# Optimization experiments

Measured on AMD Instinct MI355X. Metric: run time of the kernel, lower is better.

The kernel has to match this reference:

```python
import jax, jax.numpy as jnp
import numpy as np

KEEP_ATTN = 0.9   # 1 - attn_pdrop
KEEP_RESID = 0.9  # 1 - resid_pdrop
B, T, C, H = 2, 2048, 1024, 16


def setup_inputs() -> dict:
    key = jax.random.key(0)
    ks = jax.random.split(key, 5)
    x = jax.random.normal(ks[0], (B, T, C), jnp.float32)
    Wqkv = jax.random.normal(ks[1], (C, 3 * C), jnp.float32) / np.float32(np.sqrt(C))
    bqkv = jnp.zeros((3 * C,), jnp.float32)
    Wproj = jax.random.normal(ks[2], (C, C), jnp.float32) / np.float32(np.sqrt(C))
    bproj = jnp.zeros((C,), jnp.float32)
    # dropout keep-masks (replace the attn_pdrop_key / resid_pdrop_key args)
    attn_drop_mask = jax.random.bernoulli(ks[3], KEEP_ATTN, (B, H, T, T))
    resid_drop_mask = jax.random.bernoulli(ks[4], KEEP_RESID, (B, T, C))
    return dict(x=x, Wqkv=Wqkv, bqkv=bqkv, Wproj=Wproj, bproj=bproj,
                attn_drop_mask=attn_drop_mask, resid_drop_mask=resid_drop_mask)


def reference(x, Wqkv, bqkv, Wproj, bproj, attn_drop_mask, resid_drop_mask):
    Bx, Tx, Cx = x.shape
    Hh = attn_drop_mask.shape[1]
    hd = Cx // Hh  # head_dim
    qkv = x @ Wqkv + bqkv                              # [B,T,3C]
    q, k, v = jnp.split(qkv, 3, axis=-1)
    q = q.reshape(Bx, Tx, Hh, hd).swapaxes(1, 2)       # [B,H,T,hd]
    k = k.reshape(Bx, Tx, Hh, hd).swapaxes(1, 2)
    v = v.reshape(Bx, Tx, Hh, hd).swapaxes(1, 2)
    attn = jnp.einsum('bhqd,bhkd->bhqk', q, k) / np.float32(np.sqrt(hd))  # [B,H,T,T]
    causal = jnp.tril(jnp.ones((Tx, Tx), dtype=bool))  # lower-triangular bias
    attn = jnp.where(causal, attn, -jnp.inf)
    attn = jax.nn.softmax(attn, axis=-1)
    attn = jnp.where(attn_drop_mask, attn / np.float32(KEEP_ATTN), 0.0)
    y = jnp.einsum('bhqk,bhkd->bhqd', attn, v)         # [B,H,T,hd]
    y = y.swapaxes(1, 2).reshape(Bx, Tx, Cx)           # [B,T,C]
    y = y @ Wproj + bproj
    y = jnp.where(resid_drop_mask, y / np.float32(KEEP_RESID), 0.0)
    return y
```

## Files before the change

kernel.cpp:

```cpp
#include <hip/hip_runtime.h>
#include <cstdint>
#include <cstddef>

typedef unsigned int u32;
typedef unsigned short u16;
typedef short s8v __attribute__((ext_vector_type(8)));
typedef __bf16 bf8v __attribute__((ext_vector_type(8)));
typedef float f4v __attribute__((ext_vector_type(4)));

#define B_ 2
#define T_ 2048
#define C_ 1024
#define H_ 16
#define HD 64
#define LOG2E 1.4426950408889634f
#define SCL (0.125f * LOG2E)

__device__ __forceinline__ u16 f2bf(float f){
  u32 u = __builtin_bit_cast(u32, f);
  u += 0x7fffu + ((u >> 16) & 1u);
  return (u16)(u >> 16);
}

__device__ __forceinline__ f4v mfma16(s8v a, s8v b, f4v c){
  return __builtin_amdgcn_mfma_f32_16x16x32_bf16((bf8v)a, (bf8v)b, c, 0, 0, 0);
}

__device__ __forceinline__ void gload_lds16(const void* g, void* l){
  __builtin_amdgcn_global_load_lds((const __attribute__((address_space(1))) u32*)g,
                                   (__attribute__((address_space(3))) u32*)l,
                                   16, 0, 0);
}

__device__ __forceinline__ void barrier_keep16(){
  asm volatile("s_waitcnt vmcnt(16) lgkmcnt(0)\n\ts_barrier" ::: "memory");
}

__global__ __launch_bounds__(256) void cast_bf16_k(const float* __restrict__ in,
                                                   u16* __restrict__ out, int n8){
  int i = blockIdx.x * 256 + threadIdx.x;
  if (i >= n8) return;
  const float4* p = (const float4*)in;
  float4 a = p[i*2], b = p[i*2+1];
  uint4 o = make_uint4(
     (u32)f2bf(a.x) | ((u32)f2bf(a.y) << 16),
     (u32)f2bf(a.z) | ((u32)f2bf(a.w) << 16),
     (u32)f2bf(b.x) | ((u32)f2bf(b.y) << 16),
     (u32)f2bf(b.z) | ((u32)f2bf(b.w) << 16));
  ((uint4*)out)[i] = o;
}

__global__ __launch_bounds__(256) void tcast_k(const float* __restrict__ src,
                                               u16* __restrict__ dst, int R, int C){
  __shared__ u16 tile[64][65];
  int t = threadIdx.x;
  int c0 = blockIdx.x * 64, r0 = blockIdx.y * 64;
  int col = t & 63, rb = t >> 6;
#pragma unroll
  for (int i = 0; i < 16; i++){
    int row = rb + i*4;
    tile[row][col] = f2bf(src[(size_t)(r0+row)*C + (c0+col)]);
  }
  __syncthreads();
#pragma unroll
  for (int i = 0; i < 16; i++){
    int oc = rb + i*4;
    dst[(size_t)(c0+oc)*R + (r0+col)] = tile[col][oc];
  }
}

__global__ __launch_bounds__(256) void tv_k(const u16* __restrict__ qkv,
                                            u16* __restrict__ VT){
  __shared__ u16 tile[64][65];
  int t = threadIdx.x;
  int tt = blockIdx.x, bh = blockIdx.y;
  int b = bh >> 4, h = bh & 15;
  int col = t & 63, rb = t >> 6;
  const u16* src = qkv + (size_t)(b*T_ + tt*64)*(3*C_) + 2*C_ + h*HD;
#pragma unroll
  for (int i = 0; i < 16; i++){
    int row = rb + i*4;
    tile[row][col] = src[(size_t)row*(3*C_) + col];
  }
  __syncthreads();
  u16* dst = VT + (size_t)bh*HD*T_ + tt*64;
#pragma unroll
  for (int i = 0; i < 16; i++){
    int d = rb + i*4;
    dst[(size_t)d*T_ + col] = tile[col][d];
  }
}

template<int MODE>
__global__ __launch_bounds__(256) void gemm_k(const u16* __restrict__ A,
                        const u16* __restrict__ Bt,
                        const float* __restrict__ bias, void* __restrict__ outp,
                        const int* __restrict__ rmask,
                        int M, int N, int K){
  __shared__ __align__(16) u16 As[2][128*32];
  __shared__ __align__(16) u16 Bs[2][128*32];
  int t = threadIdx.x;
  int w = t >> 6, l = t & 63;
  int lo = l & 15, lg = l >> 4;
  int m0 = blockIdx.x * 128, n0 = blockIdx.y * 128;
  int wm = (w >> 1) * 64, wn = (w & 1) * 64;

  auto STAGE = [&](int buf, int ks){
#pragma unroll
    for (int i = 0; i < 2; i++){
      int c = t + i*256;
      int row = c >> 2, k8 = (c & 3) * 8;
      gload_lds16(A  + (size_t)(m0+row)*K + ks + k8,
                  (char*)As[buf] + (size_t)(w*64 + i*256)*16);
      gload_lds16(Bt + (size_t)(n0+row)*K + ks + k8,
                  (char*)Bs[buf] + (size_t)(w*64 + i*256)*16);
    }
  };

  f4v acc[4][4];
#pragma unroll
  for (int i=0;i<4;i++)
#pragma unroll
    for (int j=0;j<4;j++) acc[i][j] = (f4v){0.f,0.f,0.f,0.f};

  STAGE(0, 0);
  __syncthreads();
  int cur = 0;
  for (int ks = 0; ks < K; ks += 32){
    if (ks + 32 < K) STAGE(cur ^ 1, ks + 32);
    s8v af[4], bfr[4];
#pragma unroll
    for (int mt=0; mt<4; mt++)
      af[mt]  = *(const s8v*)(&As[cur][0] + (wm + mt*16 + lo)*32 + lg*8);
#pragma unroll
    for (int nt=0; nt<4; nt++)
      bfr[nt] = *(const s8v*)(&Bs[cur][0] + (wn + nt*16 + lo)*32 + lg*8);
#pragma unroll
    for (int mt=0; mt<4; mt++)
#pragma unroll
      for (int nt=0; nt<4; nt++)
        acc[mt][nt] = mfma16(af[mt], bfr[nt], acc[mt][nt]);
    __syncthreads();
    cur ^= 1;
  }

#pragma unroll
  for (int mt=0; mt<4; mt++){
#pragma unroll
    for (int nt=0; nt<4; nt++){
#pragma unroll
      for (int r=0; r<4; r++){
        int row = m0 + wm + mt*16 + lg*4 + r;
        int col = n0 + wn + nt*16 + lo;
        float v = acc[mt][nt][r] + bias[col];
        if (MODE == 0){
          ((u16*)outp)[(size_t)row*N + col] = f2bf(v);
        } else {
          float o = rmask[(size_t)row*N + col] ? v * (1.0f/0.9f) : 0.0f;
          ((float*)outp)[(size_t)row*N + col] = o;
        }
      }
    }
  }
}

__global__ __launch_bounds__(256, 4) void attn_k(const u16* __restrict__ qkv,
                        const u16* __restrict__ VT,
                        const int* __restrict__ amask,
                        u16* __restrict__ Y){
  __shared__ __align__(16) u16 Ks[2][64*64];
  __shared__ __align__(16) u16 Vs[2][64*64];
  __shared__ __align__(16) u16 Ps[4][16*64];
  const int t = threadIdx.x;
  const int w = t >> 6, l = t & 63;
  const int lo = l & 15, lg = l >> 4;

  const int n = blockIdx.x;
  const int bh = n & 31;
  const int j = n >> 5, a = j & 7, bb = j >> 3;
  const int qt = (bb & 1) ? (31 - a - 8*(bb >> 1)) : (a + 8*(bb >> 1));
  const int b = bh >> 4, h = bh & 15;
  const int q0 = qt * 64;
  const int qmaxw = q0 + w*16 + 15;

  const u16* Kg = qkv + (size_t)(b*T_)*(3*C_) + C_ + h*HD;
  const u16* Vg = VT + (size_t)bh*HD*T_;
  const int* mg = amask + (size_t)bh*T_*T_ + (size_t)(q0 + w*16)*T_;

  int qrow = q0 + w*16 + lo;
  const u16* qp = qkv + (size_t)(b*T_ + qrow)*(3*C_) + h*HD;
  s8v qf0 = *(const s8v*)(qp + lg*8);
  s8v qf1 = *(const s8v*)(qp + 32 + lg*8);

  f4v acc[4];
#pragma unroll
  for (int i=0;i<4;i++) acc[i] = (f4v){0.f,0.f,0.f,0.f};
  float lsum[4] = {0.f, 0.f, 0.f, 0.f};

  auto STAGE = [&](int buf, int kt){
#pragma unroll
    for (int i = 0; i < 2; i++){
      int c = t + i*256;
      int row = c >> 3;
      int cc = (c & 7) ^ (row & 7);
      gload_lds16(Kg + (size_t)(kt*64 + row)*(3*C_) + cc*8,
                  (char*)Ks[buf] + (size_t)(w*64 + i*256)*16);
      gload_lds16(Vg + (size_t)row*T_ + kt*64 + cc*8,
                  (char*)Vs[buf] + (size_t)(w*64 + i*256)*16);
    }
    __builtin_amdgcn_sched_barrier(0);
  };

  auto MLOAD = [&](int kt, int* m){
#pragma unroll
    for (int k4 = 0; k4 < 4; k4++)
#pragma unroll
      for (int r = 0; r < 4; r++)
        m[k4*4 + r] = mg[(size_t)(lg*4 + r)*T_ + kt*64 + k4*16 + lo];
  };

  auto TILE = [&](int kt, int cur, const int* m, bool diag){
    const char* kb = (const char*)Ks[cur];
    const char* vb = (const char*)Vs[cur];
    char* pw = (char*)&Ps[w][0];
#pragma unroll
    for (int k4 = 0; k4 < 4; k4++){
      bool active = !diag || (kt*64 + k4*16 <= qmaxw);
      f4v s = (f4v){0.f,0.f,0.f,0.f};
      if (active){
#pragma unroll
        for (int kk = 0; kk < 2; kk++){
          int krow = k4*16 + lo;
          int off = krow*128 + (((kk*4 + lg) ^ (krow & 7)) << 4);
          s8v kf = *(const s8v*)(kb + off);
          s = mfma16(kk ? qf1 : qf0, kf, s);
        }
      }
      int kidx = kt*64 + k4*16 + lo;
#pragma unroll
      for (int r=0;r<4;r++){
        float sv = active ? s[r] : -1e30f;
        if (diag){
          int qi = q0 + w*16 + lg*4 + r;
          sv = (kidx <= qi) ? sv : -1e30f;
        }
        float e = exp2f(sv * SCL);
        lsum[r] += e;
        u16 pv = m[k4*4 + r] ? f2bf(e) : (u16)0;
        int prow = lg*4 + r;
        int off = (prow*128 + (k4*16 + lo)*2) ^ ((prow & 7) << 4);
        *(u16*)(pw + off) = pv;
      }
    }
    s8v pf[2];
#pragma unroll
    for (int kk=0;kk<2;kk++){
      int off = lo*128 + (((kk*4 + lg) ^ (lo & 7)) << 4);
      pf[kk] = *(const s8v*)(pw + off);
    }
#pragma unroll
    for (int dt=0; dt<4; dt++){
#pragma unroll
      for (int kk=0; kk<2; kk++){
        int vrow = dt*16 + lo;
        int voff = vrow*128 + (((kk*4 + lg) ^ (vrow & 7)) << 4);
        s8v vf = *(const s8v*)(vb + voff);
        acc[dt] = mfma16(pf[kk], vf, acc[dt]);
      }
    }
  };

  int mA[16], mB[16];
  STAGE(0, 0);
  MLOAD(0, mA);
  __syncthreads();

  int cur = 0;
  int kt = 0;
  for (; kt + 1 < qt; kt += 2){
    STAGE(cur ^ 1, kt + 1);
    MLOAD(kt + 1, mB);
    TILE(kt, cur, mA, false);
    barrier_keep16();
    cur ^= 1;

    STAGE(cur ^ 1, kt + 2);
    MLOAD(kt + 2, mA);
    TILE(kt + 1, cur, mB, false);
    barrier_keep16();
    cur ^= 1;
  }
  if (kt < qt){
    STAGE(cur ^ 1, kt + 1);
    MLOAD(kt + 1, mB);
    TILE(kt, cur, mA, false);
    barrier_keep16();
    cur ^= 1;
    TILE(qt, cur, mB, true);
  } else {
    TILE(qt, cur, mA, true);
  }

#pragma unroll
  for (int r=0;r<4;r++){
    float v = lsum[r];
    v += __shfl_xor(v, 1);
    v += __shfl_xor(v, 2);
    v += __shfl_xor(v, 4);
    v += __shfl_xor(v, 8);
    int qi = q0 + w*16 + lg*4 + r;
    float inv = 1.0f / (v * 0.9f);
    u16* yp = Y + (size_t)(b*T_ + qi)*C_ + h*HD;
#pragma unroll
    for (int dt=0; dt<4; dt++){
      yp[dt*16 + lo] = f2bf(acc[dt][r] * inv);
    }
  }
}

extern "C" void kernel_launch(void* const* d_in, const int* in_sizes, int n_in,
                              void* d_out, int out_size, void* d_ws, size_t ws_size,
                              hipStream_t stream){
  const float* x     = (const float*)d_in[0];
  const float* Wqkv  = (const float*)d_in[1];
  const float* bqkv  = (const float*)d_in[2];
  const float* Wproj = (const float*)d_in[3];
  const float* bproj = (const float*)d_in[4];
  const int* amask = (const int*)d_in[5];
  const int* rmask = (const int*)d_in[6];
  float* out = (float*)d_out;

  char* ws = (char*)d_ws;
  u16* xb     = (u16*)(ws);
  u16* WqkvT  = (u16*)(ws + (size_t)( 8<<20));
  u16* WprojT = (u16*)(ws + (size_t)(14<<20));
  u16* qkv    = (u16*)(ws + (size_t)(16<<20));
  u16* VT     = (u16*)(ws + (size_t)(40<<20));
  u16* Yb     = (u16*)(ws + (size_t)(48<<20));

  cast_bf16_k<<<dim3(2048), dim3(256), 0, stream>>>(x, xb, (B_*T_*C_)/8);
  tcast_k<<<dim3(48, 16), dim3(256), 0, stream>>>(Wqkv, WqkvT, C_, 3*C_);
  tcast_k<<<dim3(16, 16), dim3(256), 0, stream>>>(Wproj, WprojT, C_, C_);
  gemm_k<0><<<dim3(32, 24), dim3(256), 0, stream>>>(xb, WqkvT, bqkv, qkv, nullptr,
                                                    B_*T_, 3*C_, C_);
  tv_k<<<dim3(32, 32), dim3(256), 0, stream>>>(qkv, VT);
  attn_k<<<dim3(1024), dim3(256), 0, stream>>>(qkv, VT, amask, Yb);
  gemm_k<1><<<dim3(32, 8), dim3(256), 0, stream>>>(Yb, WprojT, bproj, out, rmask,
                                                   B_*T_, C_, C_);
}
```

Measured before the change: 775.2 us.

## Load K and V fragments directly from global memory, dropping LDS staging

The attention kernel no longer stages K and V tiles into double-buffered shared memory through async global-to-LDS loads and barriers. Each wave now reads its MFMA operand fragments straight from global memory (and L2/cache). This removes the block-wide barriers and cuts LDS use, which may raise occupancy. In exchange the four waves each re-fetch the same K/V data, and loads are exposed without explicit prefetch.

Measured after the change: 874.8 us. +12.8%, slower.

```diff
diff --git a/kernel.cpp b/kernel.cpp
--- a/kernel.cpp
+++ b/kernel.cpp
@@ -30,10 +30,6 @@
   __builtin_amdgcn_global_load_lds((const __attribute__((address_space(1))) u32*)g,
                                    (__attribute__((address_space(3))) u32*)l,
                                    16, 0, 0);
-}
-
-__device__ __forceinline__ void barrier_keep16(){
-  asm volatile("s_waitcnt vmcnt(16) lgkmcnt(0)\n\ts_barrier" ::: "memory");
 }
 
 __global__ __launch_bounds__(256) void cast_bf16_k(const float* __restrict__ in,
@@ -168,8 +164,6 @@
                         const u16* __restrict__ VT,
                         const int* __restrict__ amask,
                         u16* __restrict__ Y){
-  __shared__ __align__(16) u16 Ks[2][64*64];
-  __shared__ __align__(16) u16 Vs[2][64*64];
   __shared__ __align__(16) u16 Ps[4][16*64];
   const int t = threadIdx.x;
   const int w = t >> 6, l = t & 63;
@@ -197,20 +191,6 @@
   for (int i=0;i<4;i++) acc[i] = (f4v){0.f,0.f,0.f,0.f};
   float lsum[4] = {0.f, 0.f, 0.f, 0.f};
 
-  auto STAGE = [&](int buf, int kt){
-#pragma unroll
-    for (int i = 0; i < 2; i++){
-      int c = t + i*256;
-      int row = c >> 3;
-      int cc = (c & 7) ^ (row & 7);
-      gload_lds16(Kg + (size_t)(kt*64 + row)*(3*C_) + cc*8,
-                  (char*)Ks[buf] + (size_t)(w*64 + i*256)*16);
-      gload_lds16(Vg + (size_t)row*T_ + kt*64 + cc*8,
-                  (char*)Vs[buf] + (size_t)(w*64 + i*256)*16);
-    }
-    __builtin_amdgcn_sched_barrier(0);
-  };
-
   auto MLOAD = [&](int kt, int* m){
 #pragma unroll
     for (int k4 = 0; k4 < 4; k4++)
@@ -219,20 +199,17 @@
         m[k4*4 + r] = mg[(size_t)(lg*4 + r)*T_ + kt*64 + k4*16 + lo];
   };
 
-  auto TILE = [&](int kt, int cur, const int* m, bool diag){
-    const char* kb = (const char*)Ks[cur];
-    const char* vb = (const char*)Vs[cur];
+  auto TILE = [&](int kt, const int* m, bool diag){
     char* pw = (char*)&Ps[w][0];
 #pragma unroll
     for (int k4 = 0; k4 < 4; k4++){
       bool active = !diag || (kt*64 + k4*16 <= qmaxw);
       f4v s = (f4v){0.f,0.f,0.f,0.f};
       if (active){
+        const u16* kr = Kg + (size_t)(kt*64 + k4*16 + lo)*(3*C_);
 #pragma unroll
         for (int kk = 0; kk < 2; kk++){
-          int krow = k4*16 + lo;
-          int off = krow*128 + (((kk*4 + lg) ^ (krow & 7)) << 4);
-          s8v kf = *(const s8v*)(kb + off);
+          s8v kf = *(const s8v*)(kr + kk*32 + lg*8);
           s = mfma16(kk ? qf1 : qf0, kf, s);
         }
       }
@@ -260,45 +237,31 @@
     }
 #pragma unroll
     for (int dt=0; dt<4; dt++){
+      const u16* vr = Vg + (size_t)(dt*16 + lo)*T_ + kt*64;
 #pragma unroll
       for (int kk=0; kk<2; kk++){
-        int vrow = dt*16 + lo;
-        int voff = vrow*128 + (((kk*4 + lg) ^ (vrow & 7)) << 4);
-        s8v vf = *(const s8v*)(vb + voff);
+        s8v vf = *(const s8v*)(vr + kk*32 + lg*8);
         acc[dt] = mfma16(pf[kk], vf, acc[dt]);
       }
     }
   };
 
   int mA[16], mB[16];
-  STAGE(0, 0);
   MLOAD(0, mA);
-  __syncthreads();
-
-  int cur = 0;
+
   int kt = 0;
   for (; kt + 1 < qt; kt += 2){
-    STAGE(cur ^ 1, kt + 1);
     MLOAD(kt + 1, mB);
-    TILE(kt, cur, mA, false);
-    barrier_keep16();
-    cur ^= 1;
-
-    STAGE(cur ^ 1, kt + 2);
+    TILE(kt, mA, false);
     MLOAD(kt + 2, mA);
-    TILE(kt + 1, cur, mB, false);
-    barrier_keep16();
-    cur ^= 1;
+    TILE(kt + 1, mB, false);
   }
   if (kt < qt){
-    STAGE(cur ^ 1, kt + 1);
     MLOAD(kt + 1, mB);
-    TILE(kt, cur, mA, false);
-    barrier_keep16();
-    cur ^= 1;
-    TILE(qt, cur, mB, true);
+    TILE(kt, mA, false);
+    TILE(qt, mB, true);
   } else {
-    TILE(qt, cur, mA, true);
+    TILE(qt, mA, true);
   }
 
 #pragma unroll
```
